# Kernel tuning notes

Hardware: AMD Instinct MI355X
Metric: run time of the kernel (lower is better)

Reference implementation:

```python
import jax, jax.numpy as jnp
import numpy as np

X_DIM = 512
C_DIM = 512
T = 32768
I_DIM = X_DIM + C_DIM


def setup_inputs() -> dict:
    key = jax.random.key(0)
    ks = jax.random.split(key, 9)
    s = 1.0 / np.sqrt(I_DIM)  # torch nn.Linear default init range
    def lin(kw, kb):
        w = jax.random.uniform(kw, (C_DIM, I_DIM), jnp.float32, -s, s)
        b = jax.random.uniform(kb, (C_DIM,), jnp.float32, -s, s)
        return w, b
    wf_w, wf_b = lin(ks[0], ks[1])
    wi_w, wi_b = lin(ks[2], ks[3])
    wc_w, wc_b = lin(ks[4], ks[5])
    wo_w, wo_b = lin(ks[6], ks[7])
    x_list = jax.random.normal(ks[8], (T, X_DIM), jnp.float32)
    return {"x_list": x_list, "wf_w": wf_w, "wf_b": wf_b, "wi_w": wi_w,
            "wi_b": wi_b, "wc_w": wc_w, "wc_b": wc_b, "wo_w": wo_w, "wo_b": wo_b}


def reference(x_list, wf_w, wf_b, wi_w, wi_b, wc_w, wc_b, wo_w, wo_b):
    c_dim = wf_w.shape[0]
    # Fuse the four gate projections into one GEMV per step (same math:
    # torch Linear y = i @ W.T + b, applied per gate then concatenated).
    W = jnp.concatenate([wf_w, wi_w, wc_w, wo_w], axis=0)  # [4*c_dim, i_dim]
    b = jnp.concatenate([wf_b, wi_b, wc_b, wo_b], axis=0)  # [4*c_dim]

    def step(carry, x):
        c, h = carry
        i = jnp.concatenate([x, h])          # [i_dim]
        g = W @ i + b                         # [4*c_dim]
        ff = jax.nn.sigmoid(g[:c_dim])
        ii = jax.nn.sigmoid(g[c_dim:2 * c_dim])
        cc = jnp.tanh(g[2 * c_dim:3 * c_dim])
        oo = jax.nn.sigmoid(g[3 * c_dim:])
        c = ff * c + ii * cc
        h = jnp.tanh(c) * oo
        return (c, h), None

    init = (jnp.zeros((c_dim,), x_list.dtype), jnp.zeros((c_dim,), x_list.dtype))
    (c, h), _ = jax.lax.scan(step, init, x_list)
    return (c, h)
```

## Files before the change

### kernel.cpp

```cpp
#include <hip/hip_runtime.h>
#include <hip/hip_bf16.h>
#include <cstdint>


#define T_TOTAL 32768
#define NBLK 64

__device__ __forceinline__ float sigm(float x) {
    return 1.0f / (1.0f + __expf(-x));
}
__device__ __forceinline__ float tanh_fast(float x) {
    float ax = fabsf(x);
    float e = __expf(2.0f * ax);
    float t = 1.0f - 2.0f / (e + 1.0f);
    return copysignf(t, x);
}

__global__ __launch_bounds__(256, 1) void lstm_gemm_x(
    const float* __restrict__ x,
    const float* __restrict__ wf, const float* __restrict__ wi,
    const float* __restrict__ wc, const float* __restrict__ wo,
    const float* __restrict__ bf, const float* __restrict__ bi,
    const float* __restrict__ bc, const float* __restrict__ bo,
    float* __restrict__ gx, int t0, int tend)
{
    __shared__ float xs[16][512];
    const int tid = threadIdx.x;
    const int tt0 = t0 + blockIdx.x * 16;
    const int j0  = blockIdx.y * 128;

    #pragma unroll
    for (int i = 0; i < 8; ++i) {
        int idx  = tid + i * 256;
        int trow = idx >> 7, kq = idx & 127;
        int t    = tt0 + trow;
        float4 v = make_float4(0.f, 0.f, 0.f, 0.f);
        if (t < tend) v = *(const float4*)(x + (size_t)t * 512 + kq * 4);
        *(float4*)&xs[trow][kq * 4] = v;
    }
    __syncthreads();

    const int j  = j0 + (tid & 127);
    const int th = tid >> 7;
    const int g  = j >> 9;
    const int jg = j & 511;
    const float* Wg = (g == 0) ? wf : (g == 1) ? wi : (g == 2) ? wc : wo;
    const float* Bg = (g == 0) ? bf : (g == 1) ? bi : (g == 2) ? bc : bo;
    const float* wrow = Wg + (size_t)jg * 1024;

    float acc[8];
    #pragma unroll
    for (int i = 0; i < 8; ++i) acc[i] = 0.f;

    for (int k = 0; k < 512; k += 4) {
        float4 w4 = *(const float4*)(wrow + k);
        #pragma unroll
        for (int tt = 0; tt < 8; ++tt) {
            float4 x4 = *(const float4*)&xs[th * 8 + tt][k];
            acc[tt] = fmaf(w4.x, x4.x, acc[tt]);
            acc[tt] = fmaf(w4.y, x4.y, acc[tt]);
            acc[tt] = fmaf(w4.z, x4.z, acc[tt]);
            acc[tt] = fmaf(w4.w, x4.w, acc[tt]);
        }
    }

    const float bias = Bg[jg];
    const int   obase = (jg >> 3) * 32 + (jg & 7) * 4 + g;
    #pragma unroll
    for (int tt = 0; tt < 8; ++tt) {
        int t = tt0 + th * 8 + tt;
        if (t < tend) gx[(size_t)(t - t0) * 2048 + obase] = acc[tt] + bias;
    }
}

__global__ __launch_bounds__(256, 1) void lstm_serial(
    const float* __restrict__ wf, const float* __restrict__ wi,
    const float* __restrict__ wc, const float* __restrict__ wo,
    const float* __restrict__ gx,
    unsigned long long* __restrict__ hdq,
    float* __restrict__ cstate,
    int t0, int steps, float* __restrict__ out)
{
    __shared__ alignas(16) float4 wlds4[4096];
    __shared__ alignas(16) float  hl[2][512];
    const int b   = blockIdx.x;
    const int tid = threadIdx.x;
    const int r   = tid >> 5;
    const int seg = tid & 31;
    const int w   = tid >> 6;
    const int l   = tid & 63;

    #pragma unroll
    for (int k = 0; k < 16; ++k) {
        int idx = k * 256 + tid;
        int ll  = idx & 63;
        int jj  = (idx >> 6) & 3;
        int gg  = (idx >> 8) & 3;
        int ww  = idx >> 10;
        const float* Wp = (gg == 0) ? wf : (gg == 1) ? wi : (gg == 2) ? wc : wo;
        int row = b * 8 + ww * 2 + (ll >> 5);
        wlds4[idx] = *(const float4*)(Wp + (size_t)row * 1024 + 512
                                      + 4 * (ll & 31) + 128 * jj);
    }
    float cold = cstate[b * 8 + r];
    __syncthreads();

    const float4* hl4  = (const float4*)hl;
    const int     wbase = w * 1024 + l;

    for (int s = 0; s < steps; ++s) {
        const int t  = t0 + s;
        const int sp = (t & 1) ^ 1;
        const int sc = t & 1;

        float4 gx4 = make_float4(0.f, 0.f, 0.f, 0.f);
        if (seg == 0)
            gx4 = *(const float4*)(gx + (size_t)s * 2048 + b * 32 + r * 4);

        float4 w00 = wlds4[wbase +   0], w01 = wlds4[wbase +  64];
        float4 w02 = wlds4[wbase + 128], w03 = wlds4[wbase + 192];
        float4 w10 = wlds4[wbase + 256], w11 = wlds4[wbase + 320];
        float4 w12 = wlds4[wbase + 384], w13 = wlds4[wbase + 448];
        float4 w20 = wlds4[wbase + 512], w21 = wlds4[wbase + 576];
        float4 w22 = wlds4[wbase + 640], w23 = wlds4[wbase + 704];
        float4 w30 = wlds4[wbase + 768], w31 = wlds4[wbase + 832];
        float4 w32 = wlds4[wbase + 896], w33 = wlds4[wbase + 960];

        if (tid < 64) {
            const unsigned need = (unsigned)t;
            const unsigned long long* src =
                hdq + (size_t)sp * 1024 + (tid >> 3) * 16 + (tid & 7);
            unsigned long long v0, v1, v2, v3, v4, v5, v6, v7;
            int guard = 0;
            bool ok = false;
            do {
                v0 = __hip_atomic_load(src,       __ATOMIC_RELAXED, __HIP_MEMORY_SCOPE_AGENT);
                v1 = __hip_atomic_load(src + 128, __ATOMIC_RELAXED, __HIP_MEMORY_SCOPE_AGENT);
                v2 = __hip_atomic_load(src + 256, __ATOMIC_RELAXED, __HIP_MEMORY_SCOPE_AGENT);
                v3 = __hip_atomic_load(src + 384, __ATOMIC_RELAXED, __HIP_MEMORY_SCOPE_AGENT);
                v4 = __hip_atomic_load(src + 512, __ATOMIC_RELAXED, __HIP_MEMORY_SCOPE_AGENT);
                v5 = __hip_atomic_load(src + 640, __ATOMIC_RELAXED, __HIP_MEMORY_SCOPE_AGENT);
                v6 = __hip_atomic_load(src + 768, __ATOMIC_RELAXED, __HIP_MEMORY_SCOPE_AGENT);
                v7 = __hip_atomic_load(src + 896, __ATOMIC_RELAXED, __HIP_MEMORY_SCOPE_AGENT);
                ok = ((unsigned)(v0 >> 32) == need) & ((unsigned)(v1 >> 32) == need)
                   & ((unsigned)(v2 >> 32) == need) & ((unsigned)(v3 >> 32) == need)
                   & ((unsigned)(v4 >> 32) == need) & ((unsigned)(v5 >> 32) == need)
                   & ((unsigned)(v6 >> 32) == need) & ((unsigned)(v7 >> 32) == need);
            } while (!ok && ++guard < (1 << 20));
            hl[sp][tid]       = __uint_as_float((unsigned)v0);
            hl[sp][tid + 64]  = __uint_as_float((unsigned)v1);
            hl[sp][tid + 128] = __uint_as_float((unsigned)v2);
            hl[sp][tid + 192] = __uint_as_float((unsigned)v3);
            hl[sp][tid + 256] = __uint_as_float((unsigned)v4);
            hl[sp][tid + 320] = __uint_as_float((unsigned)v5);
            hl[sp][tid + 384] = __uint_as_float((unsigned)v6);
            hl[sp][tid + 448] = __uint_as_float((unsigned)v7);
        }
        __syncthreads();

        float4 h0 = hl4[sp * 128 + seg];
        float4 h1 = hl4[sp * 128 + seg + 32];
        float4 h2 = hl4[sp * 128 + seg + 64];
        float4 h3 = hl4[sp * 128 + seg + 96];

        float a0 = 0.f, a1 = 0.f, a2 = 0.f, a3 = 0.f;
        a0 = fmaf(w00.x, h0.x, a0); a0 = fmaf(w00.y, h0.y, a0);
        a0 = fmaf(w00.z, h0.z, a0); a0 = fmaf(w00.w, h0.w, a0);
        a0 = fmaf(w01.x, h1.x, a0); a0 = fmaf(w01.y, h1.y, a0);
        a0 = fmaf(w01.z, h1.z, a0); a0 = fmaf(w01.w, h1.w, a0);
        a0 = fmaf(w02.x, h2.x, a0); a0 = fmaf(w02.y, h2.y, a0);
        a0 = fmaf(w02.z, h2.z, a0); a0 = fmaf(w02.w, h2.w, a0);
        a0 = fmaf(w03.x, h3.x, a0); a0 = fmaf(w03.y, h3.y, a0);
        a0 = fmaf(w03.z, h3.z, a0); a0 = fmaf(w03.w, h3.w, a0);

        a1 = fmaf(w10.x, h0.x, a1); a1 = fmaf(w10.y, h0.y, a1);
        a1 = fmaf(w10.z, h0.z, a1); a1 = fmaf(w10.w, h0.w, a1);
        a1 = fmaf(w11.x, h1.x, a1); a1 = fmaf(w11.y, h1.y, a1);
        a1 = fmaf(w11.z, h1.z, a1); a1 = fmaf(w11.w, h1.w, a1);
        a1 = fmaf(w12.x, h2.x, a1); a1 = fmaf(w12.y, h2.y, a1);
        a1 = fmaf(w12.z, h2.z, a1); a1 = fmaf(w12.w, h2.w, a1);
        a1 = fmaf(w13.x, h3.x, a1); a1 = fmaf(w13.y, h3.y, a1);
        a1 = fmaf(w13.z, h3.z, a1); a1 = fmaf(w13.w, h3.w, a1);

        a2 = fmaf(w20.x, h0.x, a2); a2 = fmaf(w20.y, h0.y, a2);
        a2 = fmaf(w20.z, h0.z, a2); a2 = fmaf(w20.w, h0.w, a2);
        a2 = fmaf(w21.x, h1.x, a2); a2 = fmaf(w21.y, h1.y, a2);
        a2 = fmaf(w21.z, h1.z, a2); a2 = fmaf(w21.w, h1.w, a2);
        a2 = fmaf(w22.x, h2.x, a2); a2 = fmaf(w22.y, h2.y, a2);
        a2 = fmaf(w22.z, h2.z, a2); a2 = fmaf(w22.w, h2.w, a2);
        a2 = fmaf(w23.x, h3.x, a2); a2 = fmaf(w23.y, h3.y, a2);
        a2 = fmaf(w23.z, h3.z, a2); a2 = fmaf(w23.w, h3.w, a2);

        a3 = fmaf(w30.x, h0.x, a3); a3 = fmaf(w30.y, h0.y, a3);
        a3 = fmaf(w30.z, h0.z, a3); a3 = fmaf(w30.w, h0.w, a3);
        a3 = fmaf(w31.x, h1.x, a3); a3 = fmaf(w31.y, h1.y, a3);
        a3 = fmaf(w31.z, h1.z, a3); a3 = fmaf(w31.w, h1.w, a3);
        a3 = fmaf(w32.x, h2.x, a3); a3 = fmaf(w32.y, h2.y, a3);
        a3 = fmaf(w32.z, h2.z, a3); a3 = fmaf(w32.w, h2.w, a3);
        a3 = fmaf(w33.x, h3.x, a3); a3 = fmaf(w33.y, h3.y, a3);
        a3 = fmaf(w33.z, h3.z, a3); a3 = fmaf(w33.w, h3.w, a3);

        #pragma unroll
        for (int m = 1; m < 32; m <<= 1) {
            a0 += __shfl_xor(a0, m);
            a1 += __shfl_xor(a1, m);
            a2 += __shfl_xor(a2, m);
            a3 += __shfl_xor(a3, m);
        }

        if (seg == 0) {
            float ff  = sigm(a0 + gx4.x);
            float iiv = sigm(a1 + gx4.y);
            float ccv = tanh_fast(a2 + gx4.z);
            float ov  = sigm(a3 + gx4.w);
            cold = fmaf(ff, cold, iiv * ccv);
            float hnew = tanh_fast(cold) * ov;
            unsigned long long tv = ((unsigned long long)(unsigned)(t + 1) << 32)
                                  | (unsigned long long)__float_as_uint(hnew);
            __hip_atomic_store(hdq + (size_t)sc * 1024 + b * 16 + r, tv,
                               __ATOMIC_RELAXED, __HIP_MEMORY_SCOPE_AGENT);
            if (t == T_TOTAL - 1) {
                out[b * 8 + r]       = cold;
                out[512 + b * 8 + r] = hnew;
            }
        }
    }

    if (seg == 0) cstate[b * 8 + r] = cold;
}

extern "C" void kernel_launch(void* const* d_in, const int* in_sizes, int n_in,
                              void* d_out, int out_size, void* d_ws, size_t ws_size,
                              hipStream_t stream)
{
    const float* x  = (const float*)d_in[0];
    const float* wf = (const float*)d_in[1];
    const float* bf = (const float*)d_in[2];
    const float* wi = (const float*)d_in[3];
    const float* bi = (const float*)d_in[4];
    const float* wc = (const float*)d_in[5];
    const float* bc = (const float*)d_in[6];
    const float* wo = (const float*)d_in[7];
    const float* bo = (const float*)d_in[8];
    float* out = (float*)d_out;

    char* wsb = (char*)d_ws;
    unsigned long long* hdq = (unsigned long long*)wsb;
    float* cst = (float*)(wsb + 16384);
    const size_t metaBytes = 16384 + 2048;
    float* gxbuf = (float*)(wsb + metaBytes);

    size_t gxCapSteps = (ws_size > metaBytes)
                        ? (ws_size - metaBytes) / (2048 * sizeof(float)) : 0;
    int CH = (gxCapSteps < (size_t)T_TOTAL) ? (int)gxCapSteps : T_TOTAL;
    CH &= ~15;
    if (CH < 16) CH = 16;

    hipMemsetAsync(wsb, 0, metaBytes, stream);

    for (int t0 = 0; t0 < T_TOTAL; t0 += CH) {
        int tend  = t0 + CH; if (tend > T_TOTAL) tend = T_TOTAL;
        int steps = tend - t0;
        dim3 ggrid((steps + 15) / 16, 16);
        lstm_gemm_x<<<ggrid, 256, 0, stream>>>(x, wf, wi, wc, wo,
                                               bf, bi, bc, bo, gxbuf, t0, tend);
        lstm_serial<<<NBLK, 256, 0, stream>>>(wf, wi, wc, wo, gxbuf,
                                              hdq, cst, t0, steps, out);
    }
}
```

Measured before the change: 68.41 ms.

## Fuse input projection into the serial recurrent kernel, dropping the precomputed gate buffer

Removes the separate batched GEMM that precomputed input-gate contributions and instead computes W_x·x_t inside the persistent recurrent kernel, before the spin-wait for h. Both the x-part and h-part weight slices are kept in LDS (64 KB each). This eliminates the large gx workspace, its write/read traffic and the chunked multi-launch loop. The x projection work overlaps with waiting on the cross-block h exchange. The cost is doubling the per-step LDS weight reads and FMAs on the serial critical path, plus a global load of x each step.

```diff
diff --git a/kernel.cpp b/kernel.cpp
--- a/kernel.cpp
+++ b/kernel.cpp
@@ -16,73 +16,23 @@
     return copysignf(t, x);
 }
 
-__global__ __launch_bounds__(256, 1) void lstm_gemm_x(
+#define FMA4(a, wv, vv) \
+    a = fmaf((wv).x, (vv).x, a); a = fmaf((wv).y, (vv).y, a); \
+    a = fmaf((wv).z, (vv).z, a); a = fmaf((wv).w, (vv).w, a)
+
+__global__ __launch_bounds__(256, 1) void lstm_fused(
     const float* __restrict__ x,
     const float* __restrict__ wf, const float* __restrict__ wi,
     const float* __restrict__ wc, const float* __restrict__ wo,
     const float* __restrict__ bf, const float* __restrict__ bi,
     const float* __restrict__ bc, const float* __restrict__ bo,
-    float* __restrict__ gx, int t0, int tend)
+    unsigned long long* __restrict__ hdq,
+    float* __restrict__ out)
 {
-    __shared__ float xs[16][512];
-    const int tid = threadIdx.x;
-    const int tt0 = t0 + blockIdx.x * 16;
-    const int j0  = blockIdx.y * 128;
+    __shared__ alignas(16) float4 whlds4[4096];
+    __shared__ alignas(16) float4 wxlds4[4096];
+    __shared__ alignas(16) float  hl[2][512];
 
-    #pragma unroll
-    for (int i = 0; i < 8; ++i) {
-        int idx  = tid + i * 256;
-        int trow = idx >> 7, kq = idx & 127;
-        int t    = tt0 + trow;
-        float4 v = make_float4(0.f, 0.f, 0.f, 0.f);
-        if (t < tend) v = *(const float4*)(x + (size_t)t * 512 + kq * 4);
-        *(float4*)&xs[trow][kq * 4] = v;
-    }
-    __syncthreads();
-
-    const int j  = j0 + (tid & 127);
-    const int th = tid >> 7;
-    const int g  = j >> 9;
-    const int jg = j & 511;
-    const float* Wg = (g == 0) ? wf : (g == 1) ? wi : (g == 2) ? wc : wo;
-    const float* Bg = (g == 0) ? bf : (g == 1) ? bi : (g == 2) ? bc : bo;
-    const float* wrow = Wg + (size_t)jg * 1024;
-
-    float acc[8];
-    #pragma unroll
-    for (int i = 0; i < 8; ++i) acc[i] = 0.f;
-
-    for (int k = 0; k < 512; k += 4) {
-        float4 w4 = *(const float4*)(wrow + k);
-        #pragma unroll
-        for (int tt = 0; tt < 8; ++tt) {
-            float4 x4 = *(const float4*)&xs[th * 8 + tt][k];
-            acc[tt] = fmaf(w4.x, x4.x, acc[tt]);
-            acc[tt] = fmaf(w4.y, x4.y, acc[tt]);
-            acc[tt] = fmaf(w4.z, x4.z, acc[tt]);
-            acc[tt] = fmaf(w4.w, x4.w, acc[tt]);
-        }
-    }
-
-    const float bias = Bg[jg];
-    const int   obase = (jg >> 3) * 32 + (jg & 7) * 4 + g;
-    #pragma unroll
-    for (int tt = 0; tt < 8; ++tt) {
-        int t = tt0 + th * 8 + tt;
-        if (t < tend) gx[(size_t)(t - t0) * 2048 + obase] = acc[tt] + bias;
-    }
-}
-
-__global__ __launch_bounds__(256, 1) void lstm_serial(
-    const float* __restrict__ wf, const float* __restrict__ wi,
-    const float* __restrict__ wc, const float* __restrict__ wo,
-    const float* __restrict__ gx,
-    unsigned long long* __restrict__ hdq,
-    float* __restrict__ cstate,
-    int t0, int steps, float* __restrict__ out)
-{
-    __shared__ alignas(16) float4 wlds4[4096];
-    __shared__ alignas(16) float  hl[2][512];
     const int b   = blockIdx.x;
     const int tid = threadIdx.x;
     const int r   = tid >> 5;
@@ -91,43 +41,54 @@
     const int l   = tid & 63;
 
     #pragma unroll
-    for (int k = 0; k < 16; ++k) {
-        int idx = k * 256 + tid;
-        int ll  = idx & 63;
-        int jj  = (idx >> 6) & 3;
-        int gg  = (idx >> 8) & 3;
-        int ww  = idx >> 10;
+    for (int k = 0; k < 32; ++k) {
+        int idx  = k * 256 + tid;
+        int sel  = idx >> 12;
+        int idx2 = idx & 4095;
+        int ll   = idx2 & 63;
+        int jj   = (idx2 >> 6) & 3;
+        int gg   = (idx2 >> 8) & 3;
+        int ww   = idx2 >> 10;
         const float* Wp = (gg == 0) ? wf : (gg == 1) ? wi : (gg == 2) ? wc : wo;
-        int row = b * 8 + ww * 2 + (ll >> 5);
-        wlds4[idx] = *(const float4*)(Wp + (size_t)row * 1024 + 512
-                                      + 4 * (ll & 31) + 128 * jj);
+        int row  = b * 8 + ww * 2 + (ll >> 5);
+        int col  = 4 * (ll & 31) + 128 * jj + (sel ? 0 : 512);
+        float4 v = *(const float4*)(Wp + (size_t)row * 1024 + col);
+        if (sel) wxlds4[idx2] = v; else whlds4[idx2] = v;
     }
-    float cold = cstate[b * 8 + r];
+    const int row = b * 8 + r;
+    float4 bias4 = make_float4(bf[row], bi[row], bc[row], bo[row]);
+
+    float cold = 0.f;
     __syncthreads();
 
-    const float4* hl4  = (const float4*)hl;
+    const float4* hl4   = (const float4*)hl;
     const int     wbase = w * 1024 + l;
 
-    for (int s = 0; s < steps; ++s) {
-        const int t  = t0 + s;
-        const int sp = (t & 1) ^ 1;
-        const int sc = t & 1;
+    for (int s = 0; s < T_TOTAL; ++s) {
+        const int sp = (s & 1) ^ 1;
+        const int sc = s & 1;
 
-        float4 gx4 = make_float4(0.f, 0.f, 0.f, 0.f);
-        if (seg == 0)
-            gx4 = *(const float4*)(gx + (size_t)s * 2048 + b * 32 + r * 4);
+        const float4* xp = (const float4*)(x + (size_t)s * 512);
+        float4 xv0 = xp[seg], xv1 = xp[seg + 32],
+               xv2 = xp[seg + 64], xv3 = xp[seg + 96];
 
-        float4 w00 = wlds4[wbase +   0], w01 = wlds4[wbase +  64];
-        float4 w02 = wlds4[wbase + 128], w03 = wlds4[wbase + 192];
-        float4 w10 = wlds4[wbase + 256], w11 = wlds4[wbase + 320];
-        float4 w12 = wlds4[wbase + 384], w13 = wlds4[wbase + 448];
-        float4 w20 = wlds4[wbase + 512], w21 = wlds4[wbase + 576];
-        float4 w22 = wlds4[wbase + 640], w23 = wlds4[wbase + 704];
-        float4 w30 = wlds4[wbase + 768], w31 = wlds4[wbase + 832];
-        float4 w32 = wlds4[wbase + 896], w33 = wlds4[wbase + 960];
+        float4 x00 = wxlds4[wbase +   0], x01 = wxlds4[wbase +  64];
+        float4 x02 = wxlds4[wbase + 128], x03 = wxlds4[wbase + 192];
+        float4 x10 = wxlds4[wbase + 256], x11 = wxlds4[wbase + 320];
+        float4 x12 = wxlds4[wbase + 384], x13 = wxlds4[wbase + 448];
+        float4 x20 = wxlds4[wbase + 512], x21 = wxlds4[wbase + 576];
+        float4 x22 = wxlds4[wbase + 640], x23 = wxlds4[wbase + 704];
+        float4 x30 = wxlds4[wbase + 768], x31 = wxlds4[wbase + 832];
+        float4 x32 = wxlds4[wbase + 896], x33 = wxlds4[wbase + 960];
+
+        float a0 = 0.f, a1 = 0.f, a2 = 0.f, a3 = 0.f;
+        FMA4(a0, x00, xv0); FMA4(a0, x01, xv1); FMA4(a0, x02, xv2); FMA4(a0, x03, xv3);
+        FMA4(a1, x10, xv0); FMA4(a1, x11, xv1); FMA4(a1, x12, xv2); FMA4(a1, x13, xv3);
+        FMA4(a2, x20, xv0); FMA4(a2, x21, xv1); FMA4(a2, x22, xv2); FMA4(a2, x23, xv3);
+        FMA4(a3, x30, xv0); FMA4(a3, x31, xv1); FMA4(a3, x32, xv2); FMA4(a3, x33, xv3);
 
         if (tid < 64) {
-            const unsigned need = (unsigned)t;
+            const unsigned need = (unsigned)s;
             const unsigned long long* src =
                 hdq + (size_t)sp * 1024 + (tid >> 3) * 16 + (tid & 7);
             unsigned long long v0, v1, v2, v3, v4, v5, v6, v7;
@@ -163,42 +124,19 @@
         float4 h2 = hl4[sp * 128 + seg + 64];
         float4 h3 = hl4[sp * 128 + seg + 96];
 
-        float a0 = 0.f, a1 = 0.f, a2 = 0.f, a3 = 0.f;
-        a0 = fmaf(w00.x, h0.x, a0); a0 = fmaf(w00.y, h0.y, a0);
-        a0 = fmaf(w00.z, h0.z, a0); a0 = fmaf(w00.w, h0.w, a0);
-        a0 = fmaf(w01.x, h1.x, a0); a0 = fmaf(w01.y, h1.y, a0);
-        a0 = fmaf(w01.z, h1.z, a0); a0 = fmaf(w01.w, h1.w, a0);
-        a0 = fmaf(w02.x, h2.x, a0); a0 = fmaf(w02.y, h2.y, a0);
-        a0 = fmaf(w02.z, h2.z, a0); a0 = fmaf(w02.w, h2.w, a0);
-        a0 = fmaf(w03.x, h3.x, a0); a0 = fmaf(w03.y, h3.y, a0);
-        a0 = fmaf(w03.z, h3.z, a0); a0 = fmaf(w03.w, h3.w, a0);
+        float4 w00 = whlds4[wbase +   0], w01 = whlds4[wbase +  64];
+        float4 w02 = whlds4[wbase + 128], w03 = whlds4[wbase + 192];
+        float4 w10 = whlds4[wbase + 256], w11 = whlds4[wbase + 320];
+        float4 w12 = whlds4[wbase + 384], w13 = whlds4[wbase + 448];
+        float4 w20 = whlds4[wbase + 512], w21 = whlds4[wbase + 576];
+        float4 w22 = whlds4[wbase + 640], w23 = whlds4[wbase + 704];
+        float4 w30 = whlds4[wbase + 768], w31 = whlds4[wbase + 832];
+        float4 w32 = whlds4[wbase + 896], w33 = whlds4[wbase + 960];
 
-        a1 = fmaf(w10.x, h0.x, a1); a1 = fmaf(w10.y, h0.y, a1);
-        a1 = fmaf(w10.z, h0.z, a1); a1 = fmaf(w10.w, h0.w, a1);
-        a1 = fmaf(w11.x, h1.x, a1); a1 = fmaf(w11.y, h1.y, a1);
-        a1 = fmaf(w11.z, h1.z, a1); a1 = fmaf(w11.w, h1.w, a1);
-        a1 = fmaf(w12.x, h2.x, a1); a1 = fmaf(w12.y, h2.y, a1);
-        a1 = fmaf(w12.z, h2.z, a1); a1 = fmaf(w12.w, h2.w, a1);
-        a1 = fmaf(w13.x, h3.x, a1); a1 = fmaf(w13.y, h3.y, a1);
-        a1 = fmaf(w13.z, h3.z, a1); a1 = fmaf(w13.w, h3.w, a1);
-
-        a2 = fmaf(w20.x, h0.x, a2); a2 = fmaf(w20.y, h0.y, a2);
-        a2 = fmaf(w20.z, h0.z, a2); a2 = fmaf(w20.w, h0.w, a2);
-        a2 = fmaf(w21.x, h1.x, a2); a2 = fmaf(w21.y, h1.y, a2);
-        a2 = fmaf(w21.z, h1.z, a2); a2 = fmaf(w21.w, h1.w, a2);
-        a2 = fmaf(w22.x, h2.x, a2); a2 = fmaf(w22.y, h2.y, a2);
-        a2 = fmaf(w22.z, h2.z, a2); a2 = fmaf(w22.w, h2.w, a2);
-        a2 = fmaf(w23.x, h3.x, a2); a2 = fmaf(w23.y, h3.y, a2);
-        a2 = fmaf(w23.z, h3.z, a2); a2 = fmaf(w23.w, h3.w, a2);
-
-        a3 = fmaf(w30.x, h0.x, a3); a3 = fmaf(w30.y, h0.y, a3);
-        a3 = fmaf(w30.z, h0.z, a3); a3 = fmaf(w30.w, h0.w, a3);
-        a3 = fmaf(w31.x, h1.x, a3); a3 = fmaf(w31.y, h1.y, a3);
-        a3 = fmaf(w31.z, h1.z, a3); a3 = fmaf(w31.w, h1.w, a3);
-        a3 = fmaf(w32.x, h2.x, a3); a3 = fmaf(w32.y, h2.y, a3);
-        a3 = fmaf(w32.z, h2.z, a3); a3 = fmaf(w32.w, h2.w, a3);
-        a3 = fmaf(w33.x, h3.x, a3); a3 = fmaf(w33.y, h3.y, a3);
-        a3 = fmaf(w33.z, h3.z, a3); a3 = fmaf(w33.w, h3.w, a3);
+        FMA4(a0, w00, h0); FMA4(a0, w01, h1); FMA4(a0, w02, h2); FMA4(a0, w03, h3);
+        FMA4(a1, w10, h0); FMA4(a1, w11, h1); FMA4(a1, w12, h2); FMA4(a1, w13, h3);
+        FMA4(a2, w20, h0); FMA4(a2, w21, h1); FMA4(a2, w22, h2); FMA4(a2, w23, h3);
+        FMA4(a3, w30, h0); FMA4(a3, w31, h1); FMA4(a3, w32, h2); FMA4(a3, w33, h3);
 
         #pragma unroll
         for (int m = 1; m < 32; m <<= 1) {
@@ -209,24 +147,22 @@
         }
 
         if (seg == 0) {
-            float ff  = sigm(a0 + gx4.x);
-            float iiv = sigm(a1 + gx4.y);
-            float ccv = tanh_fast(a2 + gx4.z);
-            float ov  = sigm(a3 + gx4.w);
+            float ff  = sigm(a0 + bias4.x);
+            float iiv = sigm(a1 + bias4.y);
+            float ccv = tanh_fast(a2 + bias4.z);
+            float ov  = sigm(a3 + bias4.w);
             cold = fmaf(ff, cold, iiv * ccv);
             float hnew = tanh_fast(cold) * ov;
-            unsigned long long tv = ((unsigned long long)(unsigned)(t + 1) << 32)
+            unsigned long long tv = ((unsigned long long)(unsigned)(s + 1) << 32)
                                   | (unsigned long long)__float_as_uint(hnew);
             __hip_atomic_store(hdq + (size_t)sc * 1024 + b * 16 + r, tv,
                                __ATOMIC_RELAXED, __HIP_MEMORY_SCOPE_AGENT);
-            if (t == T_TOTAL - 1) {
-                out[b * 8 + r]       = cold;
-                out[512 + b * 8 + r] = hnew;
+            if (s == T_TOTAL - 1) {
+                out[row]       = cold;
+                out[512 + row] = hnew;
             }
         }
     }
-
-    if (seg == 0) cstate[b * 8 + r] = cold;
 }
 
 extern "C" void kernel_launch(void* const* d_in, const int* in_sizes, int n_in,
@@ -244,27 +180,10 @@
     const float* bo = (const float*)d_in[8];
     float* out = (float*)d_out;
 
-    char* wsb = (char*)d_ws;
-    unsigned long long* hdq = (unsigned long long*)wsb;
-    float* cst = (float*)(wsb + 16384);
-    const size_t metaBytes = 16384 + 2048;
-    float* gxbuf = (float*)(wsb + metaBytes);
+    unsigned long long* hdq = (unsigned long long*)d_ws;
 
-    size_t gxCapSteps = (ws_size > metaBytes)
-                        ? (ws_size - metaBytes) / (2048 * sizeof(float)) : 0;
-    int CH = (gxCapSteps < (size_t)T_TOTAL) ? (int)gxCapSteps : T_TOTAL;
-    CH &= ~15;
-    if (CH < 16) CH = 16;
+    hipMemsetAsync(d_ws, 0, 16384, stream);
 
-    hipMemsetAsync(wsb, 0, metaBytes, stream);
-
-    for (int t0 = 0; t0 < T_TOTAL; t0 += CH) {
-        int tend  = t0 + CH; if (tend > T_TOTAL) tend = T_TOTAL;
-        int steps = tend - t0;
-        dim3 ggrid((steps + 15) / 16, 16);
-        lstm_gemm_x<<<ggrid, 256, 0, stream>>>(x, wf, wi, wc, wo,
-                                               bf, bi, bc, bo, gxbuf, t0, tend);
-        lstm_serial<<<NBLK, 256, 0, stream>>>(wf, wi, wc, wo, gxbuf,
-                                              hdq, cst, t0, steps, out);
-    }
+    lstm_fused<<<NBLK, 256, 0, stream>>>(x, wf, wi, wc, wo,
+                                         bf, bi, bc, bo, hdq, out);
 }
```

Result: slower. 73.65 ms (+7.7%).
